# Kernel optimization log

Hardware: AMD Instinct MI355X
Metric: run time of the kernel (lower is better)

Reference implementation:

```python
import jax, jax.numpy as jnp
import numpy as np

V_PATCH_NUMS = (1, 2, 4, 6, 8, 10, 13, 16)
HW = 16
QUANT_RESI = 0.5
SHARE_K = 4
BETA = 1.0


def _pool_matrix(n_in, n_out):
    # adaptive average pooling as a [n_out, n_in] matrix (matches F.adaptive_avg_pool2d bins)
    P = np.zeros((n_out, n_in), np.float32)
    for i in range(n_out):
        s = (i * n_in) // n_out
        e = -((-(i + 1) * n_in) // n_out)  # ceil((i+1)*n_in/n_out)
        P[i, s:e] = 1.0 / (e - s)
    return jnp.asarray(P)


def _phi_index(si, SN):
    # PhiPartiallyShared.__getitem__(si/(SN-1)) with K=4 ticks
    K = SHARE_K
    ticks = np.linspace(1.0 / 3 / K, 1 - 1.0 / 3 / K, K) if K == 4 else np.linspace(1.0 / 2 / K, 1 - 1.0 / 2 / K, K)
    return int(np.argmin(np.abs(ticks - si / (SN - 1))))


def _phi(h, w, b):
    # Phi: h*(1-r) + conv3x3(h)*r, zero padding (nn.Conv2d default)
    y = jax.lax.conv_general_dilated(h, w, (1, 1), 'SAME',
                                     dimension_numbers=('NCHW', 'OIHW', 'NCHW'))
    y = y + b[None, :, None, None]
    return h * (1.0 - QUANT_RESI) + y * QUANT_RESI


def setup_inputs() -> dict:
    key = jax.random.key(0)
    k0, k1, k2 = jax.random.split(key, 3)
    B, C, V = 64, 32, 4096
    f = jax.random.normal(k0, (B, C, HW, HW), jnp.float32)
    embed = jax.random.normal(k1, (V, C), jnp.float32)  # EMAEmbedding.weight ~ randn
    phi_w = jax.random.normal(k2, (SHARE_K, C, C, 3, 3), jnp.float32) * (1.0 / np.sqrt(9.0 * C))
    phi_b = jnp.zeros((SHARE_K, C), jnp.float32)
    return {"f_BChw": f, "embed_weight": embed, "phi_w": phi_w, "phi_b": phi_b}


def reference(f_BChw, embed_weight, phi_w, phi_b):
    B, C, H, W = f_BChw.shape
    SN = len(V_PATCH_NUMS)
    f_ng = jax.lax.stop_gradient(f_BChw)
    f_hat = jnp.zeros_like(f_BChw)
    e_sq = jnp.sum(embed_weight * embed_weight, axis=1)  # [V]
    loss = jnp.float32(0.0)
    for si, pn in enumerate(V_PATCH_NUMS):
        rest = f_ng - jax.lax.stop_gradient(f_hat)  # residual to quantize (no grad through distance)
        if pn != H:
            P = _pool_matrix(H, pn)
            rest_d = jnp.einsum('oh,bchw,pw->bcop', P, rest, P)  # adaptive avg pool -> [B,C,pn,pn]
        else:
            rest_d = rest
        rest_NC = rest_d.transpose(0, 2, 3, 1).reshape(-1, C)  # [B*pn*pn, C]
        # squared euclidean cdist to codebook, argmin
        d = (jnp.sum(rest_NC * rest_NC, axis=1, keepdims=True)
             + e_sq[None, :]
             - 2.0 * (rest_NC @ embed_weight.T))  # [N, V]
        idx = jnp.argmin(d, axis=1)  # [B*pn*pn] int
        h = embed_weight[idx].reshape(B, pn, pn, C).transpose(0, 3, 1, 2)  # gather -> [B,C,pn,pn]
        if pn != H:
            h = jax.image.resize(h, (B, C, H, W), method='linear')  # bilinear, align_corners=False
        k = _phi_index(si, SN)
        h = _phi(h, phi_w[k], phi_b[k])
        f_hat = f_hat + h
        loss = loss + 0.25 * jnp.mean((jax.lax.stop_gradient(f_hat) - f_BChw) ** 2) \
                    + BETA * jnp.mean((f_hat - f_ng) ** 2)
    loss = loss / SN
    # straight-through estimator: grads flow to f_BChw as identity
    f_hat_st = jax.lax.stop_gradient(f_hat - f_BChw) + f_BChw
    return f_hat_st, loss
```

## Files before the change

kernel.cpp:

```cpp
#include <hip/hip_runtime.h>
#include <hip/hip_bf16.h>

#define BB 64
#define CC 32
#define HW2 256
#define VV 4096
#define NELEM (BB*CC*HW2)
#define PADW 18
#define PADA 324

#define OFF_F     0
#define OFF_FHAT  (OFF_F     + NELEM)
#define OFF_EMBT  (OFF_FHAT  + NELEM)
#define OFF_ESQ   (OFF_EMBT  + VV*CC)
#define OFF_PW    (OFF_ESQ   + VV)
#define OFF_PB    (OFF_PW    + 4*CC*CC*9)
#define OFF_REST  (OFF_PB    + 4*CC)
#define OFF_BESTA (OFF_REST  + 16384*CC)
#define OFF_BESTB (OFF_BESTA + 2*16384)
#define OFF_LOSS  (OFF_BESTB + 2*16384)
#define OFF_FLAG  (OFF_LOSS  + 1)

__device__ __forceinline__ int embt_idx(int v, int c) {
    return (v >> 6) * 2048 + c * 64 + (v & 63);
}

__global__ void k_probe(const void* __restrict__ fin, int* __restrict__ flag) {
    __shared__ int cnt[256];
    int t = threadIdx.x;
    const __hip_bfloat16* p = (const __hip_bfloat16*)fin;
    int local = 0;
    for (int i = t; i < 8192; i += 256) {
        float v = __bfloat162float(p[i]);
        if (!(fabsf(v) < 1e3f)) local++;
    }
    cnt[t] = local;
    __syncthreads();
    for (int s = 128; s > 0; s >>= 1) {
        if (t < s) cnt[t] += cnt[t + s];
        __syncthreads();
    }
    if (t == 0) *flag = (cnt[0] >= 64) ? 1 : 0;
}

__global__ void k_prep(const void* __restrict__ fin,
                       const void* __restrict__ ein,
                       const void* __restrict__ win,
                       const void* __restrict__ bin_,
                       const int* __restrict__ flag,
                       float* __restrict__ f, float* __restrict__ fhat,
                       float* __restrict__ embT, float* __restrict__ pw,
                       float* __restrict__ pb, float* __restrict__ loss) {
    bool isf32 = (*flag != 0);
    int i = blockIdx.x * 256 + threadIdx.x;
    if (i < NELEM) {
        f[i] = isf32 ? ((const float*)fin)[i]
                     : __bfloat162float(((const __hip_bfloat16*)fin)[i]);
        fhat[i] = 0.f;
    }
    if (i < VV*CC) {
        float ev = isf32 ? ((const float*)ein)[i]
                         : __bfloat162float(((const __hip_bfloat16*)ein)[i]);
        int v = i >> 5, c = i & 31;
        embT[embt_idx(v, c)] = ev;
    }
    if (i < 4*CC*CC*9)
        pw[i] = isf32 ? ((const float*)win)[i]
                      : __bfloat162float(((const __hip_bfloat16*)win)[i]);
    if (i < 4*CC)
        pb[i] = isf32 ? ((const float*)bin_)[i]
                      : __bfloat162float(((const __hip_bfloat16*)bin_)[i]);
    if (i == 0) *loss = 0.f;
}

__global__ void k_esq(const float* __restrict__ embT, float* __restrict__ esq) {
    int v = blockIdx.x * 256 + threadIdx.x;
    if (v >= VV) return;
    const float* p = embT + (v >> 6) * 2048 + (v & 63);
    float s = 0.f;
    #pragma unroll
    for (int c = 0; c < CC; ++c) { float e = p[c * 64]; s = fmaf(e, e, s); }
    esq[v] = s;
}

__global__ void k_pool0(const float* __restrict__ f, const float* __restrict__ fhat,
                        float* __restrict__ rest, unsigned long long* __restrict__ best) {
    int n = threadIdx.x;
    int c = blockIdx.y;
    if (n >= BB) return;
    if (c == 0) best[n] = 0xFFFFFFFFFFFFFFFFull;
    const float* fb = f + (n * CC + c) * HW2;
    const float* hb = fhat + (n * CC + c) * HW2;
    float s = 0.f;
    for (int h = 0; h < 16; ++h)
        for (int w = 0; w < 16; ++w)
            s += fb[h * 16 + w] - hb[h * 16 + w];
    rest[n * CC + c] = s * (1.f / 256.f);
}

__global__ __launch_bounds__(256)
void k_argmin(const float* __restrict__ rest, const float* __restrict__ embT,
              const float* __restrict__ esq, unsigned long long* __restrict__ best,
              int Ntot, int cpw) {
    __shared__ float xT[CC][132];
    __shared__ float eT[CC * 64];
    __shared__ float xxs[2][128];
    int tid = threadIdx.x;
    int tx = tid & 15, ty = tid >> 4;
    int qblk = blockIdx.x * 128;
    int v0 = blockIdx.y * cpw;
    int t0 = v0 >> 6;

    {
        int q = tid >> 1, h = tid & 1;
        int qq = qblk + q; if (qq > Ntot - 1) qq = Ntot - 1;
        const float* xr = rest + qq * CC + h * 16;
        float part = 0.f;
        #pragma unroll
        for (int c = 0; c < 16; ++c) {
            float xv = xr[c];
            xT[h * 16 + c][q] = xv;
            part = fmaf(xv, xv, part);
        }
        xxs[h][q] = part;
    }
    __syncthreads();

    float xx[8];
    #pragma unroll
    for (int i = 0; i < 8; ++i) {
        int q = ty * 8 + i;
        xx[i] = xxs[0][q] + xxs[1][q];
    }

    float bd[8]; int bi[8];
    #pragma unroll
    for (int i = 0; i < 8; ++i) { bd[i] = 3.4e38f; bi[i] = v0; }

    int ntiles = cpw >> 6;
    for (int t = 0; t < ntiles; ++t) {
        int vbase = v0 + t * 64;
        const float* gt = embT + (size_t)(t0 + t) * 2048;
        float4 s0 = *(const float4*)(gt + tid * 4);
        float4 s1 = *(const float4*)(gt + 1024 + tid * 4);
        __syncthreads();
        *(float4*)(eT + tid * 4) = s0;
        *(float4*)(eT + 1024 + tid * 4) = s1;
        __syncthreads();

        float acc[8][4];
        #pragma unroll
        for (int i = 0; i < 8; ++i)
            #pragma unroll
            for (int j = 0; j < 4; ++j) acc[i][j] = 0.f;

        #pragma unroll 8
        for (int k = 0; k < CC; ++k) {
            float a[8], b[4];
            #pragma unroll
            for (int i = 0; i < 8; ++i) a[i] = xT[k][ty * 8 + i];
            #pragma unroll
            for (int j = 0; j < 4; ++j) b[j] = eT[k * 64 + tx * 4 + j];
            #pragma unroll
            for (int i = 0; i < 8; ++i)
                #pragma unroll
                for (int j = 0; j < 4; ++j)
                    acc[i][j] = fmaf(a[i], b[j], acc[i][j]);
        }

        float4 es4 = *(const float4*)(esq + vbase + tx * 4);
        float es[4] = {es4.x, es4.y, es4.z, es4.w};
        #pragma unroll
        for (int i = 0; i < 8; ++i) {
            float base = xx[i];
            #pragma unroll
            for (int j = 0; j < 4; ++j) {
                float dist = fmaf(-2.f, acc[i][j], base + es[j]);
                if (dist < bd[i]) { bd[i] = dist; bi[i] = vbase + tx * 4 + j; }
            }
        }
    }

    #pragma unroll
    for (int i = 0; i < 8; ++i) {
        unsigned u = __float_as_uint(bd[i]);
        unsigned long long mono = (u & 0x80000000u)
            ? (unsigned long long)(~u)
            : (unsigned long long)(u | 0x80000000u);
        unsigned long long pk = (mono << 32) | (unsigned long long)(unsigned)bi[i];
        #pragma unroll
        for (int m = 1; m <= 8; m <<= 1) {
            unsigned long long o = __shfl_xor(pk, m, 64);
            if (o < pk) pk = o;
        }
        int q = qblk + ty * 8 + i;
        if (tx == 0 && q < Ntot)
            atomicMin(best + q, pk);
    }
}

__global__ __launch_bounds__(512)
void k_fuse(const float* __restrict__ embT,
            const unsigned long long* __restrict__ best,
            const float* __restrict__ pw, const float* __restrict__ pb,
            const float* __restrict__ f, float* __restrict__ fhat,
            float* __restrict__ loss,
            float* __restrict__ rest,
            unsigned long long* __restrict__ best_next,
            int pn, int k, int pn_next) {
    __shared__ float h_pad[CC * PADA];
    __shared__ float extra[CC * 169];
    __shared__ float red[8];
    int b = blockIdx.x, coq = blockIdx.y, t = threadIdx.x;
    int nn = pn * pn;
    int pix = t & 255, half = t >> 8;
    int y = pix >> 4, x = pix & 15;
    int c0 = half * 16;

    for (int i = t; i < CC * PADA; i += 512) h_pad[i] = 0.f;

    if (pn == 16) {
        __syncthreads();
        int id = (int)(unsigned)(best[b * HW2 + pix] & 0xFFFFFFFFull);
        const float* er = embT + (id >> 6) * 2048 + (id & 63);
        int ctr = (y + 1) * PADW + (x + 1);
        #pragma unroll
        for (int c = 0; c < 16; ++c)
            h_pad[(c0 + c) * PADA + ctr] = er[(c0 + c) * 64];
    } else {
        float (*hs)[169] = (float(*)[169])extra;
        for (int cell = t; cell < nn; cell += 512) {
            int id = (int)(unsigned)(best[b * nn + cell] & 0xFFFFFFFFull);
            const float* er = embT + (id >> 6) * 2048 + (id & 63);
            #pragma unroll
            for (int c = 0; c < CC; ++c) hs[c][cell] = er[c * 64];
        }
        __syncthreads();
        float scale = (float)pn / 16.f;
        float sy = (y + 0.5f) * scale - 0.5f;
        sy = fminf(fmaxf(sy, 0.f), (float)(pn - 1));
        int y0 = (int)sy; int y1 = min(y0 + 1, pn - 1); float wy = sy - (float)y0;
        float sx = (x + 0.5f) * scale - 0.5f;
        sx = fminf(fmaxf(sx, 0.f), (float)(pn - 1));
        int x0 = (int)sx; int x1 = min(x0 + 1, pn - 1); float wx = sx - (float)x0;
        float wy0 = 1.f - wy, wx0 = 1.f - wx;
        int ctr = (y + 1) * PADW + (x + 1);
        #pragma unroll
        for (int c = 0; c < 16; ++c) {
            int cc = c0 + c;
            float v00 = hs[cc][y0 * pn + x0], v01 = hs[cc][y0 * pn + x1];
            float v10 = hs[cc][y1 * pn + x0], v11 = hs[cc][y1 * pn + x1];
            float a0 = wy0 * v00 + wy * v10;
            float a1 = wy0 * v01 + wy * v11;
            h_pad[cc * PADA + ctr] = wx0 * a0 + wx * a1;
        }
    }
    __syncthreads();

    float acc[4];
    #pragma unroll
    for (int o = 0; o < 4; ++o) acc[o] = 0.f;
    const float* hbase = h_pad + y * PADW + x;
    const float* wpk = pw + (k * CC + coq * 8 + half * 4) * (CC * 9);
    #pragma unroll
    for (int ci_ = 0; ci_ < CC; ++ci_) {
        float hv[9];
        #pragma unroll
        for (int dy = 0; dy < 3; ++dy)
            #pragma unroll
            for (int dx = 0; dx < 3; ++dx)
                hv[dy * 3 + dx] = hbase[ci_ * PADA + dy * PADW + dx];
        const float* wp = wpk + ci_ * 9;
        #pragma unroll
        for (int o = 0; o < 4; ++o) {
            const float* w9 = wp + o * (CC * 9);
            #pragma unroll
            for (int q = 0; q < 9; ++q) acc[o] = fmaf(hv[q], w9[q], acc[o]);
        }
    }

    float* diff = extra;
    float lsum = 0.f;
    int ctr = (y + 1) * PADW + (x + 1);
    #pragma unroll
    for (int o = 0; o < 4; ++o) {
        int lo = half * 4 + o;
        int co = coq * 8 + lo;
        float hval = h_pad[co * PADA + ctr];
        float outv = hval * 0.5f + (acc[o] + pb[k * CC + co]) * 0.5f;
        int pos = (b * CC + co) * HW2 + pix;
        float fh = fhat[pos] + outv;
        fhat[pos] = fh;
        float dd = f[pos] - fh;
        diff[lo * HW2 + pix] = dd;
        lsum = fmaf(dd, dd, lsum);
    }
    #pragma unroll
    for (int off = 32; off > 0; off >>= 1) lsum += __shfl_down(lsum, off, 64);
    if ((t & 63) == 0) red[t >> 6] = lsum;
    __syncthreads();
    if (t == 0) {
        float s = 0.f;
        #pragma unroll
        for (int w = 0; w < 8; ++w) s += red[w];
        atomicAdd(loss, s);
    }

    if (pn_next > 0) {
        int nn2 = pn_next * pn_next;
        for (int q = t; q < nn2 * 8; q += 512) {
            int cell = q % nn2, o = q / nn2;
            int i = cell / pn_next, j = cell % pn_next;
            int s0 = (i * 16) / pn_next, e0 = ((i + 1) * 16 + pn_next - 1) / pn_next;
            int s1 = (j * 16) / pn_next, e1 = ((j + 1) * 16 + pn_next - 1) / pn_next;
            float inv = 1.f / (float)((e0 - s0) * (e1 - s1));
            float s = 0.f;
            for (int h = s0; h < e0; ++h)
                for (int w = s1; w < e1; ++w)
                    s += diff[o * HW2 + h * 16 + w];
            rest[(b * nn2 + cell) * CC + coq * 8 + o] = s * inv;
        }
        if (coq == 0)
            for (int q = t; q < nn2; q += 512)
                best_next[b * nn2 + q] = 0xFFFFFFFFFFFFFFFFull;
    }
}

__global__ void k_out(const float* __restrict__ fhat, const float* __restrict__ loss,
                      const int* __restrict__ flag, void* __restrict__ out) {
    bool isf32 = (*flag != 0);
    int i = blockIdx.x * 256 + threadIdx.x;
    if (i > NELEM) return;
    float v;
    if (i < NELEM) v = fhat[i];
    else           v = (*loss) * (1.25f / (float)NELEM / 8.f);
    if (isf32) ((float*)out)[i] = v;
    else       ((__hip_bfloat16*)out)[i] = __float2bfloat16(v);
}

extern "C" void kernel_launch(void* const* d_in, const int* in_sizes, int n_in,
                              void* d_out, int out_size, void* d_ws, size_t ws_size,
                              hipStream_t stream) {
    const void* fin  = d_in[0];
    const void* ein  = d_in[1];
    const void* win  = d_in[2];
    const void* bin_ = d_in[3];
    float* ws = (float*)d_ws;
    float* f    = ws + OFF_F;
    float* fhat = ws + OFF_FHAT;
    float* embT = ws + OFF_EMBT;
    float* esq  = ws + OFF_ESQ;
    float* pw   = ws + OFF_PW;
    float* pb   = ws + OFF_PB;
    float* rest = ws + OFF_REST;
    unsigned long long* bestA = (unsigned long long*)(ws + OFF_BESTA);
    unsigned long long* bestB = (unsigned long long*)(ws + OFF_BESTB);
    float* loss = ws + OFF_LOSS;
    int*   flag = (int*)(ws + OFF_FLAG);

    static const int PN[8] = {1, 2, 4, 6, 8, 10, 13, 16};
    static const int KK[8] = {0, 0, 1, 1, 2, 2, 3, 3};
    static const int SP[8] = {64, 64, 64, 64, 32, 32, 16, 16};

    k_probe<<<1, 256, 0, stream>>>(fin, flag);
    k_prep<<<(NELEM + 255) / 256, 256, 0, stream>>>(fin, ein, win, bin_, flag, f, fhat, embT, pw, pb, loss);
    k_esq<<<(VV + 255) / 256, 256, 0, stream>>>(embT, esq);
    k_pool0<<<dim3(1, CC), 256, 0, stream>>>(f, fhat, rest, bestA);

    for (int si = 0; si < 8; ++si) {
        int pn = PN[si];
        int Ntot = BB * pn * pn;
        int Sp = SP[si];
        int cpw = VV / Sp;
        unsigned long long* bcur = (si & 1) ? bestB : bestA;
        unsigned long long* bnxt = (si & 1) ? bestA : bestB;
        int pn_next = (si < 7) ? PN[si + 1] : 0;
        int gx = (Ntot + 127) / 128;
        k_argmin<<<dim3(gx, Sp), 256, 0, stream>>>(rest, embT, esq, bcur, Ntot, cpw);
        k_fuse<<<dim3(BB, 4), 512, 0, stream>>>(embT, bcur, pw, pb, f, fhat, loss,
                                                rest, bnxt, pn, KK[si], pn_next);
    }
    k_out<<<(NELEM + 1 + 255) / 256, 256, 0, stream>>>(fhat, loss, flag, d_out);
}
```

Before: 500.7 us.

## Fuse all quantization stages into one persistent kernel with grid barriers

Replaces the per-scale chain of argmin and fuse kernel launches (plus esq, pool0 and output kernels) with a single persistent kernel of 256 blocks that steps through the stages and separates them with atomic-counter grid barriers. The argmin tiling is widened to 256 queries per unit with float4 shared-memory reads, and the codebook split factors are retuned per scale. This removes launch overhead and inter-kernel gaps, but relies on all 256 blocks being co-resident, and spin barriers can hang or add latency if they are not.

```diff
diff --git a/kernel.cpp b/kernel.cpp
--- a/kernel.cpp
+++ b/kernel.cpp
@@ -8,6 +8,8 @@
 #define NELEM (BB*CC*HW2)
 #define PADW 18
 #define PADA 324
+#define NBLK 256
+#define NTHR 512
 
 #define OFF_F     0
 #define OFF_FHAT  (OFF_F     + NELEM)
@@ -20,6 +22,7 @@
 #define OFF_BESTB (OFF_BESTA + 2*16384)
 #define OFF_LOSS  (OFF_BESTB + 2*16384)
 #define OFF_FLAG  (OFF_LOSS  + 1)
+#define OFF_BAR   (OFF_FLAG  + 1)
 
 __device__ __forceinline__ int embt_idx(int v, int c) {
     return (v >> 6) * 2048 + c * 64 + (v & 63);
@@ -50,7 +53,8 @@
                        const int* __restrict__ flag,
                        float* __restrict__ f, float* __restrict__ fhat,
                        float* __restrict__ embT, float* __restrict__ pw,
-                       float* __restrict__ pb, float* __restrict__ loss) {
+                       float* __restrict__ pb, float* __restrict__ loss,
+                       int* __restrict__ bar) {
     bool isf32 = (*flag != 0);
     int i = blockIdx.x * 256 + threadIdx.x;
     if (i < NELEM) {
@@ -70,272 +74,296 @@
     if (i < 4*CC)
         pb[i] = isf32 ? ((const float*)bin_)[i]
                       : __bfloat162float(((const __hip_bfloat16*)bin_)[i]);
+    if (i < 32) bar[i] = 0;
     if (i == 0) *loss = 0.f;
 }
 
-__global__ void k_esq(const float* __restrict__ embT, float* __restrict__ esq) {
-    int v = blockIdx.x * 256 + threadIdx.x;
-    if (v >= VV) return;
-    const float* p = embT + (v >> 6) * 2048 + (v & 63);
-    float s = 0.f;
-    #pragma unroll
-    for (int c = 0; c < CC; ++c) { float e = p[c * 64]; s = fmaf(e, e, s); }
-    esq[v] = s;
-}
-
-__global__ void k_pool0(const float* __restrict__ f, const float* __restrict__ fhat,
-                        float* __restrict__ rest, unsigned long long* __restrict__ best) {
-    int n = threadIdx.x;
-    int c = blockIdx.y;
-    if (n >= BB) return;
-    if (c == 0) best[n] = 0xFFFFFFFFFFFFFFFFull;
-    const float* fb = f + (n * CC + c) * HW2;
-    const float* hb = fhat + (n * CC + c) * HW2;
-    float s = 0.f;
-    for (int h = 0; h < 16; ++h)
-        for (int w = 0; w < 16; ++w)
-            s += fb[h * 16 + w] - hb[h * 16 + w];
-    rest[n * CC + c] = s * (1.f / 256.f);
-}
-
-__global__ __launch_bounds__(256)
-void k_argmin(const float* __restrict__ rest, const float* __restrict__ embT,
-              const float* __restrict__ esq, unsigned long long* __restrict__ best,
-              int Ntot, int cpw) {
-    __shared__ float xT[CC][132];
-    __shared__ float eT[CC * 64];
-    __shared__ float xxs[2][128];
-    int tid = threadIdx.x;
-    int tx = tid & 15, ty = tid >> 4;
-    int qblk = blockIdx.x * 128;
-    int v0 = blockIdx.y * cpw;
-    int t0 = v0 >> 6;
+__device__ __forceinline__ void gsync(int* bar, int idx) {
+    __threadfence();
+    __syncthreads();
+    if (threadIdx.x == 0) {
+        atomicAdd(&bar[idx], 1);
+        while (atomicAdd(&bar[idx], 0) < NBLK) __builtin_amdgcn_s_sleep(2);
+    }
+    __syncthreads();
+    __threadfence();
+}
+
+__global__ __launch_bounds__(NTHR, 2)
+void k_persist(float* __restrict__ rest, const float* __restrict__ embT,
+               float* __restrict__ esq,
+               unsigned long long* __restrict__ bestA,
+               unsigned long long* __restrict__ bestB,
+               const float* __restrict__ pw, const float* __restrict__ pb,
+               const float* __restrict__ f, float* __restrict__ fhat,
+               float* __restrict__ loss, const int* __restrict__ flag,
+               void* __restrict__ out, int* __restrict__ bar) {
+    __shared__ __align__(16) float smem[15784];
+    float (*xT)[260] = (float(*)[260])smem;
+    float* eT  = smem + 8320;
+    float* xxs = smem + 10368;
+    float* h_pad = smem;
+    float* extra = smem + 10368;
+    float* red   = smem + 15776;
+
+    const int PNa[8] = {1, 2, 4, 6, 8, 10, 13, 16};
+    const int SPa[8] = {64, 64, 64, 32, 16, 8, 8, 4};
+    const int KKa[8] = {0, 0, 1, 1, 2, 2, 3, 3};
+
+    int blk = blockIdx.x, t = threadIdx.x;
 
     {
-        int q = tid >> 1, h = tid & 1;
-        int qq = qblk + q; if (qq > Ntot - 1) qq = Ntot - 1;
-        const float* xr = rest + qq * CC + h * 16;
-        float part = 0.f;
-        #pragma unroll
-        for (int c = 0; c < 16; ++c) {
-            float xv = xr[c];
-            xT[h * 16 + c][q] = xv;
-            part = fmaf(xv, xv, part);
+        int g = blk * NTHR + t;
+        if (g < VV) {
+            const float* p = embT + (g >> 6) * 2048 + (g & 63);
+            float s = 0.f;
+            #pragma unroll
+            for (int c = 0; c < CC; ++c) { float e = p[c * 64]; s = fmaf(e, e, s); }
+            esq[g] = s;
         }
-        xxs[h][q] = part;
-    }
-    __syncthreads();
-
-    float xx[8];
-    #pragma unroll
-    for (int i = 0; i < 8; ++i) {
-        int q = ty * 8 + i;
-        xx[i] = xxs[0][q] + xxs[1][q];
-    }
-
-    float bd[8]; int bi[8];
-    #pragma unroll
-    for (int i = 0; i < 8; ++i) { bd[i] = 3.4e38f; bi[i] = v0; }
-
-    int ntiles = cpw >> 6;
-    for (int t = 0; t < ntiles; ++t) {
-        int vbase = v0 + t * 64;
-        const float* gt = embT + (size_t)(t0 + t) * 2048;
-        float4 s0 = *(const float4*)(gt + tid * 4);
-        float4 s1 = *(const float4*)(gt + 1024 + tid * 4);
-        __syncthreads();
-        *(float4*)(eT + tid * 4) = s0;
-        *(float4*)(eT + 1024 + tid * 4) = s1;
-        __syncthreads();
-
-        float acc[8][4];
-        #pragma unroll
-        for (int i = 0; i < 8; ++i)
-            #pragma unroll
-            for (int j = 0; j < 4; ++j) acc[i][j] = 0.f;
-
-        #pragma unroll 8
-        for (int k = 0; k < CC; ++k) {
-            float a[8], b[4];
-            #pragma unroll
-            for (int i = 0; i < 8; ++i) a[i] = xT[k][ty * 8 + i];
-            #pragma unroll
-            for (int j = 0; j < 4; ++j) b[j] = eT[k * 64 + tx * 4 + j];
-            #pragma unroll
-            for (int i = 0; i < 8; ++i)
-                #pragma unroll
-                for (int j = 0; j < 4; ++j)
-                    acc[i][j] = fmaf(a[i], b[j], acc[i][j]);
+        int p0 = g - 8192;
+        if (p0 >= 0 && p0 < BB * CC) {
+            int n = p0 >> 5, c = p0 & 31;
+            const float* fb = f + (n * CC + c) * HW2;
+            float s = 0.f;
+            for (int h = 0; h < 16; ++h)
+                for (int w = 0; w < 16; ++w)
+                    s += fb[h * 16 + w];
+            rest[n * CC + c] = s * (1.f / 256.f);
+            if (c == 0) bestA[n] = 0xFFFFFFFFFFFFFFFFull;
         }
-
-        float4 es4 = *(const float4*)(esq + vbase + tx * 4);
-        float es[4] = {es4.x, es4.y, es4.z, es4.w};
-        #pragma unroll
-        for (int i = 0; i < 8; ++i) {
-            float base = xx[i];
-            #pragma unroll
-            for (int j = 0; j < 4; ++j) {
-                float dist = fmaf(-2.f, acc[i][j], base + es[j]);
-                if (dist < bd[i]) { bd[i] = dist; bi[i] = vbase + tx * 4 + j; }
+    }
+    gsync(bar, 0);
+
+    int bidx = 1;
+    for (int si = 0; si < 8; ++si) {
+        int pn = PNa[si], Sp = SPa[si], k = KKa[si];
+        int Ntot = BB * pn * pn;
+        int gxq = (Ntot + 255) >> 8;
+        int cpw = VV / Sp;
+        int units = gxq * Sp;
+        unsigned long long* bcur = (si & 1) ? bestB : bestA;
+        unsigned long long* bnxt = (si & 1) ? bestA : bestB;
+        int pn_next = (si < 7) ? PNa[si + 1] : 0;
+
+        int tx = t & 15, ty = t >> 4;
+        for (int u = blk; u < units; u += NBLK) {
+            int qblk = (u % gxq) * 256;
+            int v0 = (u / gxq) * cpw;
+            int t0 = v0 >> 6;
+
+            __syncthreads();
+            {
+                int q = t >> 1, h = t & 1;
+                int qq = qblk + q; if (qq > Ntot - 1) qq = Ntot - 1;
+                const float* xr = rest + qq * CC + h * 16;
+                float part = 0.f;
+                #pragma unroll
+                for (int c = 0; c < 16; ++c) {
+                    float xv = xr[c];
+                    xT[h * 16 + c][q] = xv;
+                    part = fmaf(xv, xv, part);
+                }
+                xxs[h * 256 + q] = part;
+            }
+            __syncthreads();
+
+            float xx[8];
+            #pragma unroll
+            for (int i = 0; i < 8; ++i) {
+                int q = ty * 8 + i;
+                xx[i] = xxs[q] + xxs[256 + q];
+            }
+            float bd[8]; int bi[8];
+            #pragma unroll
+            for (int i = 0; i < 8; ++i) { bd[i] = 3.4e38f; bi[i] = v0; }
+
+            int ntiles = cpw >> 6;
+            for (int tt = 0; tt < ntiles; ++tt) {
+                int vbase = v0 + tt * 64;
+                float4 s0 = ((const float4*)(embT + (size_t)(t0 + tt) * 2048))[t];
+                __syncthreads();
+                ((float4*)eT)[t] = s0;
+                __syncthreads();
+
+                float acc[8][4];
+                #pragma unroll
+                for (int i = 0; i < 8; ++i)
+                    #pragma unroll
+                    for (int j = 0; j < 4; ++j) acc[i][j] = 0.f;
+
+                #pragma unroll 8
+                for (int kk = 0; kk < CC; ++kk) {
+                    float4 a0 = *(const float4*)&xT[kk][ty * 8];
+                    float4 a1 = *(const float4*)&xT[kk][ty * 8 + 4];
+                    float4 b4 = *(const float4*)&eT[kk * 64 + tx * 4];
+                    float a[8] = {a0.x, a0.y, a0.z, a0.w, a1.x, a1.y, a1.z, a1.w};
+                    float b[4] = {b4.x, b4.y, b4.z, b4.w};
+                    #pragma unroll
+                    for (int i = 0; i < 8; ++i)
+                        #pragma unroll
+                        for (int j = 0; j < 4; ++j)
+                            acc[i][j] = fmaf(a[i], b[j], acc[i][j]);
+                }
+
+                float4 es4 = *(const float4*)(esq + vbase + tx * 4);
+                float es[4] = {es4.x, es4.y, es4.z, es4.w};
+                #pragma unroll
+                for (int i = 0; i < 8; ++i) {
+                    float base = xx[i];
+                    #pragma unroll
+                    for (int j = 0; j < 4; ++j) {
+                        float dist = fmaf(-2.f, acc[i][j], base + es[j]);
+                        if (dist < bd[i]) { bd[i] = dist; bi[i] = vbase + tx * 4 + j; }
+                    }
+                }
+            }
+
+            #pragma unroll
+            for (int i = 0; i < 8; ++i) {
+                unsigned uu = __float_as_uint(bd[i]);
+                unsigned long long mono = (uu & 0x80000000u)
+                    ? (unsigned long long)(~uu)
+                    : (unsigned long long)(uu | 0x80000000u);
+                unsigned long long pk = (mono << 32) | (unsigned long long)(unsigned)bi[i];
+                #pragma unroll
+                for (int m = 1; m <= 8; m <<= 1) {
+                    unsigned long long o = __shfl_xor(pk, m, 64);
+                    if (o < pk) pk = o;
+                }
+                int q = qblk + ty * 8 + i;
+                if (tx == 0 && q < Ntot)
+                    atomicMin(bcur + q, pk);
             }
         }
-    }
-
-    #pragma unroll
-    for (int i = 0; i < 8; ++i) {
-        unsigned u = __float_as_uint(bd[i]);
-        unsigned long long mono = (u & 0x80000000u)
-            ? (unsigned long long)(~u)
-            : (unsigned long long)(u | 0x80000000u);
-        unsigned long long pk = (mono << 32) | (unsigned long long)(unsigned)bi[i];
-        #pragma unroll
-        for (int m = 1; m <= 8; m <<= 1) {
-            unsigned long long o = __shfl_xor(pk, m, 64);
-            if (o < pk) pk = o;
+        gsync(bar, bidx++);
+
+        {
+            int b = blk >> 2, coq = blk & 3;
+            int nn = pn * pn;
+            int pix = t & 255, half = t >> 8;
+            int y = pix >> 4, x = pix & 15;
+            int c0 = half * 16;
+
+            for (int i = t; i < CC * PADA; i += NTHR) h_pad[i] = 0.f;
+
+            if (pn == 16) {
+                __syncthreads();
+                int id = (int)(unsigned)(bcur[b * HW2 + pix] & 0xFFFFFFFFull);
+                const float* er = embT + (id >> 6) * 2048 + (id & 63);
+                int ctr = (y + 1) * PADW + (x + 1);
+                #pragma unroll
+                for (int c = 0; c < 16; ++c)
+                    h_pad[(c0 + c) * PADA + ctr] = er[(c0 + c) * 64];
+            } else {
+                float (*hs)[169] = (float(*)[169])extra;
+                for (int cell = t; cell < nn; cell += NTHR) {
+                    int id = (int)(unsigned)(bcur[b * nn + cell] & 0xFFFFFFFFull);
+                    const float* er = embT + (id >> 6) * 2048 + (id & 63);
+                    #pragma unroll
+                    for (int c = 0; c < CC; ++c) hs[c][cell] = er[c * 64];
+                }
+                __syncthreads();
+                float scale = (float)pn / 16.f;
+                float sy = (y + 0.5f) * scale - 0.5f;
+                sy = fminf(fmaxf(sy, 0.f), (float)(pn - 1));
+                int y0 = (int)sy; int y1 = min(y0 + 1, pn - 1); float wy = sy - (float)y0;
+                float sx = (x + 0.5f) * scale - 0.5f;
+                sx = fminf(fmaxf(sx, 0.f), (float)(pn - 1));
+                int x0 = (int)sx; int x1 = min(x0 + 1, pn - 1); float wx = sx - (float)x0;
+                float wy0 = 1.f - wy, wx0 = 1.f - wx;
+                int ctr = (y + 1) * PADW + (x + 1);
+                #pragma unroll
+                for (int c = 0; c < 16; ++c) {
+                    int cc = c0 + c;
+                    float v00 = hs[cc][y0 * pn + x0], v01 = hs[cc][y0 * pn + x1];
+                    float v10 = hs[cc][y1 * pn + x0], v11 = hs[cc][y1 * pn + x1];
+                    float a0 = wy0 * v00 + wy * v10;
+                    float a1 = wy0 * v01 + wy * v11;
+                    h_pad[cc * PADA + ctr] = wx0 * a0 + wx * a1;
+                }
+            }
+            __syncthreads();
+
+            float acc[4];
+            #pragma unroll
+            for (int o = 0; o < 4; ++o) acc[o] = 0.f;
+            const float* hbase = h_pad + y * PADW + x;
+            const float* wpk = pw + (k * CC + coq * 8 + half * 4) * (CC * 9);
+            #pragma unroll
+            for (int ci_ = 0; ci_ < CC; ++ci_) {
+                float hv[9];
+                #pragma unroll
+                for (int dy = 0; dy < 3; ++dy)
+                    #pragma unroll
+                    for (int dx = 0; dx < 3; ++dx)
+                        hv[dy * 3 + dx] = hbase[ci_ * PADA + dy * PADW + dx];
+                const float* wp = wpk + ci_ * 9;
+                #pragma unroll
+                for (int o = 0; o < 4; ++o) {
+                    const float* w9 = wp + o * (CC * 9);
+                    #pragma unroll
+                    for (int q = 0; q < 9; ++q) acc[o] = fmaf(hv[q], w9[q], acc[o]);
+                }
+            }
+
+            float* diff = extra;
+            float lsum = 0.f;
+            int ctr = (y + 1) * PADW + (x + 1);
+            #pragma unroll
+            for (int o = 0; o < 4; ++o) {
+                int lo = half * 4 + o;
+                int co = coq * 8 + lo;
+                float hval = h_pad[co * PADA + ctr];
+                float outv = hval * 0.5f + (acc[o] + pb[k * CC + co]) * 0.5f;
+                int pos = (b * CC + co) * HW2 + pix;
+                float fh = fhat[pos] + outv;
+                fhat[pos] = fh;
+                float dd = f[pos] - fh;
+                diff[lo * HW2 + pix] = dd;
+                lsum = fmaf(dd, dd, lsum);
+            }
+            #pragma unroll
+            for (int off = 32; off > 0; off >>= 1) lsum += __shfl_down(lsum, off, 64);
+            if ((t & 63) == 0) red[t >> 6] = lsum;
+            __syncthreads();
+            if (t == 0) {
+                float s = 0.f;
+                #pragma unroll
+                for (int w = 0; w < 8; ++w) s += red[w];
+                atomicAdd(loss, s);
+            }
+
+            if (pn_next > 0) {
+                int nn2 = pn_next * pn_next;
+                for (int q = t; q < nn2 * 8; q += NTHR) {
+                    int cell = q % nn2, o = q / nn2;
+                    int i = cell / pn_next, j = cell % pn_next;
+                    int s0 = (i * 16) / pn_next, e0 = ((i + 1) * 16 + pn_next - 1) / pn_next;
+                    int s1 = (j * 16) / pn_next, e1 = ((j + 1) * 16 + pn_next - 1) / pn_next;
+                    float inv = 1.f / (float)((e0 - s0) * (e1 - s1));
+                    float s = 0.f;
+                    for (int h = s0; h < e0; ++h)
+                        for (int w = s1; w < e1; ++w)
+                            s += diff[o * HW2 + h * 16 + w];
+                    rest[(b * nn2 + cell) * CC + coq * 8 + o] = s * inv;
+                }
+                if (coq == 0)
+                    for (int q = t; q < nn2; q += NTHR)
+                        bnxt[b * nn2 + q] = 0xFFFFFFFFFFFFFFFFull;
+            }
         }
-        int q = qblk + ty * 8 + i;
-        if (tx == 0 && q < Ntot)
-            atomicMin(best + q, pk);
-    }
-}
-
-__global__ __launch_bounds__(512)
-void k_fuse(const float* __restrict__ embT,
-            const unsigned long long* __restrict__ best,
-            const float* __restrict__ pw, const float* __restrict__ pb,
-            const float* __restrict__ f, float* __restrict__ fhat,
-            float* __restrict__ loss,
-            float* __restrict__ rest,
-            unsigned long long* __restrict__ best_next,
-            int pn, int k, int pn_next) {
-    __shared__ float h_pad[CC * PADA];
-    __shared__ float extra[CC * 169];
-    __shared__ float red[8];
-    int b = blockIdx.x, coq = blockIdx.y, t = threadIdx.x;
-    int nn = pn * pn;
-    int pix = t & 255, half = t >> 8;
-    int y = pix >> 4, x = pix & 15;
-    int c0 = half * 16;
-
-    for (int i = t; i < CC * PADA; i += 512) h_pad[i] = 0.f;
-
-    if (pn == 16) {
-        __syncthreads();
-        int id = (int)(unsigned)(best[b * HW2 + pix] & 0xFFFFFFFFull);
-        const float* er = embT + (id >> 6) * 2048 + (id & 63);
-        int ctr = (y + 1) * PADW + (x + 1);
-        #pragma unroll
-        for (int c = 0; c < 16; ++c)
-            h_pad[(c0 + c) * PADA + ctr] = er[(c0 + c) * 64];
-    } else {
-        float (*hs)[169] = (float(*)[169])extra;
-        for (int cell = t; cell < nn; cell += 512) {
-            int id = (int)(unsigned)(best[b * nn + cell] & 0xFFFFFFFFull);
-            const float* er = embT + (id >> 6) * 2048 + (id & 63);
-            #pragma unroll
-            for (int c = 0; c < CC; ++c) hs[c][cell] = er[c * 64];
-        }
-        __syncthreads();
-        float scale = (float)pn / 16.f;
-        float sy = (y + 0.5f) * scale - 0.5f;
-        sy = fminf(fmaxf(sy, 0.f), (float)(pn - 1));
-        int y0 = (int)sy; int y1 = min(y0 + 1, pn - 1); float wy = sy - (float)y0;
-        float sx = (x + 0.5f) * scale - 0.5f;
-        sx = fminf(fmaxf(sx, 0.f), (float)(pn - 1));
-        int x0 = (int)sx; int x1 = min(x0 + 1, pn - 1); float wx = sx - (float)x0;
-        float wy0 = 1.f - wy, wx0 = 1.f - wx;
-        int ctr = (y + 1) * PADW + (x + 1);
-        #pragma unroll
-        for (int c = 0; c < 16; ++c) {
-            int cc = c0 + c;
-            float v00 = hs[cc][y0 * pn + x0], v01 = hs[cc][y0 * pn + x1];
-            float v10 = hs[cc][y1 * pn + x0], v11 = hs[cc][y1 * pn + x1];
-            float a0 = wy0 * v00 + wy * v10;
-            float a1 = wy0 * v01 + wy * v11;
-            h_pad[cc * PADA + ctr] = wx0 * a0 + wx * a1;
-        }
-    }
-    __syncthreads();
-
-    float acc[4];
-    #pragma unroll
-    for (int o = 0; o < 4; ++o) acc[o] = 0.f;
-    const float* hbase = h_pad + y * PADW + x;
-    const float* wpk = pw + (k * CC + coq * 8 + half * 4) * (CC * 9);
-    #pragma unroll
-    for (int ci_ = 0; ci_ < CC; ++ci_) {
-        float hv[9];
-        #pragma unroll
-        for (int dy = 0; dy < 3; ++dy)
-            #pragma unroll
-            for (int dx = 0; dx < 3; ++dx)
-                hv[dy * 3 + dx] = hbase[ci_ * PADA + dy * PADW + dx];
-        const float* wp = wpk + ci_ * 9;
-        #pragma unroll
-        for (int o = 0; o < 4; ++o) {
-            const float* w9 = wp + o * (CC * 9);
-            #pragma unroll
-            for (int q = 0; q < 9; ++q) acc[o] = fmaf(hv[q], w9[q], acc[o]);
-        }
-    }
-
-    float* diff = extra;
-    float lsum = 0.f;
-    int ctr = (y + 1) * PADW + (x + 1);
-    #pragma unroll
-    for (int o = 0; o < 4; ++o) {
-        int lo = half * 4 + o;
-        int co = coq * 8 + lo;
-        float hval = h_pad[co * PADA + ctr];
-        float outv = hval * 0.5f + (acc[o] + pb[k * CC + co]) * 0.5f;
-        int pos = (b * CC + co) * HW2 + pix;
-        float fh = fhat[pos] + outv;
-        fhat[pos] = fh;
-        float dd = f[pos] - fh;
-        diff[lo * HW2 + pix] = dd;
-        lsum = fmaf(dd, dd, lsum);
-    }
-    #pragma unroll
-    for (int off = 32; off > 0; off >>= 1) lsum += __shfl_down(lsum, off, 64);
-    if ((t & 63) == 0) red[t >> 6] = lsum;
-    __syncthreads();
-    if (t == 0) {
-        float s = 0.f;
-        #pragma unroll
-        for (int w = 0; w < 8; ++w) s += red[w];
-        atomicAdd(loss, s);
-    }
-
-    if (pn_next > 0) {
-        int nn2 = pn_next * pn_next;
-        for (int q = t; q < nn2 * 8; q += 512) {
-            int cell = q % nn2, o = q / nn2;
-            int i = cell / pn_next, j = cell % pn_next;
-            int s0 = (i * 16) / pn_next, e0 = ((i + 1) * 16 + pn_next - 1) / pn_next;
-            int s1 = (j * 16) / pn_next, e1 = ((j + 1) * 16 + pn_next - 1) / pn_next;
-            float inv = 1.f / (float)((e0 - s0) * (e1 - s1));
-            float s = 0.f;
-            for (int h = s0; h < e0; ++h)
-                for (int w = s1; w < e1; ++w)
-                    s += diff[o * HW2 + h * 16 + w];
-            rest[(b * nn2 + cell) * CC + coq * 8 + o] = s * inv;
-        }
-        if (coq == 0)
-            for (int q = t; q < nn2; q += 512)
-                best_next[b * nn2 + q] = 0xFFFFFFFFFFFFFFFFull;
-    }
-}
-
-__global__ void k_out(const float* __restrict__ fhat, const float* __restrict__ loss,
-                      const int* __restrict__ flag, void* __restrict__ out) {
+        gsync(bar, bidx++);
+    }
+
     bool isf32 = (*flag != 0);
-    int i = blockIdx.x * 256 + threadIdx.x;
-    if (i > NELEM) return;
-    float v;
-    if (i < NELEM) v = fhat[i];
-    else           v = (*loss) * (1.25f / (float)NELEM / 8.f);
-    if (isf32) ((float*)out)[i] = v;
-    else       ((__hip_bfloat16*)out)[i] = __float2bfloat16(v);
+    for (int i = blk * NTHR + t; i <= NELEM; i += NBLK * NTHR) {
+        float v;
+        if (i < NELEM) v = fhat[i];
+        else           v = (*loss) * (1.25f / (float)NELEM / 8.f);
+        if (isf32) ((float*)out)[i] = v;
+        else       ((__hip_bfloat16*)out)[i] = __float2bfloat16(v);
+    }
 }
 
 extern "C" void kernel_launch(void* const* d_in, const int* in_sizes, int n_in,
@@ -357,28 +385,11 @@
     unsigned long long* bestB = (unsigned long long*)(ws + OFF_BESTB);
     float* loss = ws + OFF_LOSS;
     int*   flag = (int*)(ws + OFF_FLAG);
-
-    static const int PN[8] = {1, 2, 4, 6, 8, 10, 13, 16};
-    static const int KK[8] = {0, 0, 1, 1, 2, 2, 3, 3};
-    static const int SP[8] = {64, 64, 64, 64, 32, 32, 16, 16};
+    int*   bar  = (int*)(ws + OFF_BAR);
 
     k_probe<<<1, 256, 0, stream>>>(fin, flag);
-    k_prep<<<(NELEM + 255) / 256, 256, 0, stream>>>(fin, ein, win, bin_, flag, f, fhat, embT, pw, pb, loss);
-    k_esq<<<(VV + 255) / 256, 256, 0, stream>>>(embT, esq);
-    k_pool0<<<dim3(1, CC), 256, 0, stream>>>(f, fhat, rest, bestA);
-
-    for (int si = 0; si < 8; ++si) {
-        int pn = PN[si];
-        int Ntot = BB * pn * pn;
-        int Sp = SP[si];
-        int cpw = VV / Sp;
-        unsigned long long* bcur = (si & 1) ? bestB : bestA;
-        unsigned long long* bnxt = (si & 1) ? bestA : bestB;
-        int pn_next = (si < 7) ? PN[si + 1] : 0;
-        int gx = (Ntot + 127) / 128;
-        k_argmin<<<dim3(gx, Sp), 256, 0, stream>>>(rest, embT, esq, bcur, Ntot, cpw);
-        k_fuse<<<dim3(BB, 4), 512, 0, stream>>>(embT, bcur, pw, pb, f, fhat, loss,
-                                                rest, bnxt, pn, KK[si], pn_next);
-    }
-    k_out<<<(NELEM + 1 + 255) / 256, 256, 0, stream>>>(fhat, loss, flag, d_out);
-}
+    k_prep<<<(NELEM + 255) / 256, 256, 0, stream>>>(fin, ein, win, bin_, flag,
+                                                    f, fhat, embT, pw, pb, loss, bar);
+    k_persist<<<NBLK, NTHR, 0, stream>>>(rest, embT, esq, bestA, bestB, pw, pb,
+                                         f, fhat, loss, flag, d_out, bar);
+}
```

Measured after the change: 1.791 ms. 3.58x slower.

## Split fuse kernel into 8 channel-group blocks of 256 threads, vectorize argmin LDS loads

Applied to the files above, without the earlier changes.

The fused gather/upsample/conv kernel now launches 512 blocks of 256 threads, each handling 4 output channels, instead of 256 blocks of 512 threads handling 8. This raises block count and lowers per-block LDS pressure, but each block still gathers and interpolates all 32 channels, so that gather and bilinear work is duplicated across twice as many blocks. Separately, the argmin inner loop reads its shared-memory operands with float4 loads instead of scalar loads, reducing LDS instruction count.

```diff
diff --git a/kernel.cpp b/kernel.cpp
--- a/kernel.cpp
+++ b/kernel.cpp
@@ -156,11 +156,11 @@
 
         #pragma unroll 8
         for (int k = 0; k < CC; ++k) {
-            float a[8], b[4];
-            #pragma unroll
-            for (int i = 0; i < 8; ++i) a[i] = xT[k][ty * 8 + i];
-            #pragma unroll
-            for (int j = 0; j < 4; ++j) b[j] = eT[k * 64 + tx * 4 + j];
+            float4 a0 = *(const float4*)&xT[k][ty * 8];
+            float4 a1 = *(const float4*)&xT[k][ty * 8 + 4];
+            float4 b4 = *(const float4*)&eT[k * 64 + tx * 4];
+            float a[8] = {a0.x, a0.y, a0.z, a0.w, a1.x, a1.y, a1.z, a1.w};
+            float b[4] = {b4.x, b4.y, b4.z, b4.w};
             #pragma unroll
             for (int i = 0; i < 8; ++i)
                 #pragma unroll
@@ -199,7 +199,7 @@
     }
 }
 
-__global__ __launch_bounds__(512)
+__global__ __launch_bounds__(256)
 void k_fuse(const float* __restrict__ embT,
             const unsigned long long* __restrict__ best,
             const float* __restrict__ pw, const float* __restrict__ pb,
@@ -210,26 +210,24 @@
             int pn, int k, int pn_next) {
     __shared__ float h_pad[CC * PADA];
     __shared__ float extra[CC * 169];
-    __shared__ float red[8];
-    int b = blockIdx.x, coq = blockIdx.y, t = threadIdx.x;
+    __shared__ float red[4];
+    int b = blockIdx.x, co8 = blockIdx.y, t = threadIdx.x;
     int nn = pn * pn;
-    int pix = t & 255, half = t >> 8;
-    int y = pix >> 4, x = pix & 15;
-    int c0 = half * 16;
-
-    for (int i = t; i < CC * PADA; i += 512) h_pad[i] = 0.f;
+    int y = t >> 4, x = t & 15;
+
+    for (int i = t; i < CC * PADA; i += 256) h_pad[i] = 0.f;
 
     if (pn == 16) {
         __syncthreads();
-        int id = (int)(unsigned)(best[b * HW2 + pix] & 0xFFFFFFFFull);
+        int id = (int)(unsigned)(best[b * HW2 + t] & 0xFFFFFFFFull);
         const float* er = embT + (id >> 6) * 2048 + (id & 63);
         int ctr = (y + 1) * PADW + (x + 1);
         #pragma unroll
-        for (int c = 0; c < 16; ++c)
-            h_pad[(c0 + c) * PADA + ctr] = er[(c0 + c) * 64];
+        for (int c = 0; c < CC; ++c)
+            h_pad[c * PADA + ctr] = er[c * 64];
     } else {
         float (*hs)[169] = (float(*)[169])extra;
-        for (int cell = t; cell < nn; cell += 512) {
+        for (int cell = t; cell < nn; cell += 256) {
             int id = (int)(unsigned)(best[b * nn + cell] & 0xFFFFFFFFull);
             const float* er = embT + (id >> 6) * 2048 + (id & 63);
             #pragma unroll
@@ -246,13 +244,12 @@
         float wy0 = 1.f - wy, wx0 = 1.f - wx;
         int ctr = (y + 1) * PADW + (x + 1);
         #pragma unroll
-        for (int c = 0; c < 16; ++c) {
-            int cc = c0 + c;
-            float v00 = hs[cc][y0 * pn + x0], v01 = hs[cc][y0 * pn + x1];
-            float v10 = hs[cc][y1 * pn + x0], v11 = hs[cc][y1 * pn + x1];
+        for (int c = 0; c < CC; ++c) {
+            float v00 = hs[c][y0 * pn + x0], v01 = hs[c][y0 * pn + x1];
+            float v10 = hs[c][y1 * pn + x0], v11 = hs[c][y1 * pn + x1];
             float a0 = wy0 * v00 + wy * v10;
             float a1 = wy0 * v01 + wy * v11;
-            h_pad[cc * PADA + ctr] = wx0 * a0 + wx * a1;
+            h_pad[c * PADA + ctr] = wx0 * a0 + wx * a1;
         }
     }
     __syncthreads();
@@ -261,7 +258,7 @@
     #pragma unroll
     for (int o = 0; o < 4; ++o) acc[o] = 0.f;
     const float* hbase = h_pad + y * PADW + x;
-    const float* wpk = pw + (k * CC + coq * 8 + half * 4) * (CC * 9);
+    const float* wpk = pw + (k * CC + co8 * 4) * (CC * 9);
     #pragma unroll
     for (int ci_ = 0; ci_ < CC; ++ci_) {
         float hv[9];
@@ -284,31 +281,26 @@
     int ctr = (y + 1) * PADW + (x + 1);
     #pragma unroll
     for (int o = 0; o < 4; ++o) {
-        int lo = half * 4 + o;
-        int co = coq * 8 + lo;
+        int co = co8 * 4 + o;
         float hval = h_pad[co * PADA + ctr];
         float outv = hval * 0.5f + (acc[o] + pb[k * CC + co]) * 0.5f;
-        int pos = (b * CC + co) * HW2 + pix;
+        int pos = (b * CC + co) * HW2 + t;
         float fh = fhat[pos] + outv;
         fhat[pos] = fh;
         float dd = f[pos] - fh;
-        diff[lo * HW2 + pix] = dd;
+        diff[o * HW2 + t] = dd;
         lsum = fmaf(dd, dd, lsum);
     }
     #pragma unroll
     for (int off = 32; off > 0; off >>= 1) lsum += __shfl_down(lsum, off, 64);
     if ((t & 63) == 0) red[t >> 6] = lsum;
     __syncthreads();
-    if (t == 0) {
-        float s = 0.f;
-        #pragma unroll
-        for (int w = 0; w < 8; ++w) s += red[w];
-        atomicAdd(loss, s);
-    }
+    if (t == 0)
+        atomicAdd(loss, red[0] + red[1] + red[2] + red[3]);
 
     if (pn_next > 0) {
         int nn2 = pn_next * pn_next;
-        for (int q = t; q < nn2 * 8; q += 512) {
+        for (int q = t; q < nn2 * 4; q += 256) {
             int cell = q % nn2, o = q / nn2;
             int i = cell / pn_next, j = cell % pn_next;
             int s0 = (i * 16) / pn_next, e0 = ((i + 1) * 16 + pn_next - 1) / pn_next;
@@ -318,10 +310,10 @@
             for (int h = s0; h < e0; ++h)
                 for (int w = s1; w < e1; ++w)
                     s += diff[o * HW2 + h * 16 + w];
-            rest[(b * nn2 + cell) * CC + coq * 8 + o] = s * inv;
-        }
-        if (coq == 0)
-            for (int q = t; q < nn2; q += 512)
+            rest[(b * nn2 + cell) * CC + co8 * 4 + o] = s * inv;
+        }
+        if (co8 == 0)
+            for (int q = t; q < nn2; q += 256)
                 best_next[b * nn2 + q] = 0xFFFFFFFFFFFFFFFFull;
     }
 }
@@ -363,7 +355,8 @@
     static const int SP[8] = {64, 64, 64, 64, 32, 32, 16, 16};
 
     k_probe<<<1, 256, 0, stream>>>(fin, flag);
-    k_prep<<<(NELEM + 255) / 256, 256, 0, stream>>>(fin, ein, win, bin_, flag, f, fhat, embT, pw, pb, loss);
+    k_prep<<<(NELEM + 255) / 256, 256, 0, stream>>>(fin, ein, win, bin_, flag,
+                                                    f, fhat, embT, pw, pb, loss);
     k_esq<<<(VV + 255) / 256, 256, 0, stream>>>(embT, esq);
     k_pool0<<<dim3(1, CC), 256, 0, stream>>>(f, fhat, rest, bestA);
 
@@ -377,7 +370,7 @@
         int pn_next = (si < 7) ? PN[si + 1] : 0;
         int gx = (Ntot + 127) / 128;
         k_argmin<<<dim3(gx, Sp), 256, 0, stream>>>(rest, embT, esq, bcur, Ntot, cpw);
-        k_fuse<<<dim3(BB, 4), 512, 0, stream>>>(embT, bcur, pw, pb, f, fhat, loss,
+        k_fuse<<<dim3(BB, 8), 256, 0, stream>>>(embT, bcur, pw, pb, f, fhat, loss,
                                                 rest, bnxt, pn, KK[si], pn_next);
     }
     k_out<<<(NELEM + 1 + 255) / 256, 256, 0, stream>>>(fhat, loss, flag, d_out);
```

Measured after the change: 464.0 us (median of 2 runs). -7.3%, faster.
